# Kernel tuning notes

Measured on AMD Instinct MI355X. Metric: run time of the kernel, lower is better.

The kernel has to match this reference:

```python
import jax, jax.numpy as jnp
import numpy as np

B = 262144
DIM = 128
TD = 32        # token_dim (per-token channel dim inside attention)
NT = DIM // TD # 4 tokens from x, +1 learnable -> N = 5
N = NT + 1
H = 8          # num_heads
HD = TD // H   # head_dim = 4
DEEP = 2


def setup_inputs() -> dict:
    key = jax.random.key(0)
    ks = jax.random.split(key, 7)
    x = jax.random.normal(ks[0], (B, DIM), dtype=jnp.float32)
    token = jax.random.normal(ks[1], (1, 1, TD), dtype=jnp.float32)
    # stacked per-layer params (DEEP layers)
    qkv_w = jax.random.normal(ks[2], (DEEP, 3 * TD, TD), dtype=jnp.float32) * (TD ** -0.5)
    qkv_b = jnp.zeros((DEEP, 3 * TD), dtype=jnp.float32)
    proj_w = jax.random.normal(ks[3], (DEEP, TD, TD), dtype=jnp.float32) * (TD ** -0.5)
    proj_b = jnp.zeros((DEEP, TD), dtype=jnp.float32)
    pos_bias = jax.random.normal(ks[4], (DEEP, H, N, N), dtype=jnp.float32)
    return {"x": x, "token": token, "qkv_w": qkv_w, "qkv_b": qkv_b,
            "proj_w": proj_w, "proj_b": proj_b, "pos_bias": pos_bias}


def reference(x, token, qkv_w, qkv_b, proj_w, proj_b, pos_bias):
    scale = HD ** -0.5
    b = x.shape[0]
    # split x into NT tokens of width TD, prepend learnable token -> [B, N, TD]
    y = jnp.concatenate(
        [jnp.broadcast_to(token, (b, 1, TD)), x.reshape(b, NT, TD)], axis=1)
    for i in range(DEEP):
        qkv = y @ qkv_w[i].T + qkv_b[i]                 # [B, N, 3*TD]
        qkv = qkv.reshape(b, N, 3, H, HD)
        q = qkv[:, :, 0].transpose(0, 2, 1, 3)          # [B, H, N, HD]
        k = qkv[:, :, 1].transpose(0, 2, 1, 3)
        v = qkv[:, :, 2].transpose(0, 2, 1, 3)
        attn = jnp.einsum('bhnd,bhmd->bhnm', q, k) * scale + pos_bias[i]
        attn = jax.nn.softmax(attn, axis=-1)
        o = jnp.einsum('bhnm,bhmd->bhnd', attn, v)      # [B, H, N, HD]
        o = o.transpose(0, 2, 1, 3).reshape(b, N, TD)
        y = y + (o @ proj_w[i].T + proj_b[i])           # residual
    return y[:, 0, :]                                   # [B, TD]
```

## Files before the change

### kernel.cpp

```cpp
#include <hip/hip_runtime.h>
#include <hip/hip_bf16.h>


#define NTOK 5

typedef decltype(__builtin_amdgcn_cvt_pkrtz(0.0f, 0.0f)) half2_t;
using half8_t = __attribute__((ext_vector_type(8))) _Float16;
using f32x4 = __attribute__((ext_vector_type(4))) float;

union H2 { half2_t h; unsigned int u; };
union H8 { half8_t h; uint4 u4; unsigned int u[4]; };

__device__ __forceinline__ half2_t u2h(unsigned int x) { H2 c; c.u = x; return c.h; }
__device__ __forceinline__ unsigned int h2u(half2_t h) { H2 c; c.h = h; return c.u; }
__device__ __forceinline__ unsigned int pk(float a, float b) {
  return h2u(__builtin_amdgcn_cvt_pkrtz(a, b));
}
__device__ __forceinline__ float bf2f(unsigned short u) {
  union { unsigned int u; float f; } c; c.u = ((unsigned int)u) << 16; return c.f;
}
__device__ __forceinline__ half2_t bfpair2h2(unsigned int u) {
  union { unsigned int u; float f; } lo, hi;
  lo.u = u << 16;
  hi.u = u & 0xffff0000u;
  return __builtin_amdgcn_cvt_pkrtz(lo.f, hi.f);
}
__device__ __forceinline__ unsigned int f2bfpair(float a, float b) {
  unsigned int ua = __float_as_uint(a), ub = __float_as_uint(b);
  ua = (ua + 0x7fffu + ((ua >> 16) & 1u)) >> 16;
  ub = (ub + 0x7fffu + ((ub >> 16) & 1u)) & 0xffff0000u;
  return ua | ub;
}

__device__ __forceinline__ int detect_bf16(const unsigned int* __restrict__ p) {
  int cnt = 0;
#pragma unroll
  for (int i = 0; i < 64; ++i) {
    unsigned int e = (p[i] >> 7) & 0xffu;
    cnt += (e >= 96u && e <= 150u) ? 1 : 0;
  }
  return (cnt >= 40) ? 1 : 0;
}

__global__ void prep_kernel(const void* __restrict__ xraw,
                            const void* __restrict__ qkv_w, const void* __restrict__ qkv_b,
                            const void* __restrict__ proj_w, const void* __restrict__ proj_b,
                            const void* __restrict__ pos_b,
                            unsigned int* __restrict__ wqkv, unsigned int* __restrict__ wproj,
                            float* __restrict__ bqkv, float* __restrict__ bproj,
                            float* __restrict__ pb, int* __restrict__ flag) {
  const int t = threadIdx.x;
  const int isbf = detect_bf16((const unsigned int*)xraw);
  if (t == 0) *flag = isbf;
  if (isbf) {
    const unsigned short* qw = (const unsigned short*)qkv_w;
    const unsigned short* qb = (const unsigned short*)qkv_b;
    const unsigned short* pw = (const unsigned short*)proj_w;
    const unsigned short* pbb = (const unsigned short*)proj_b;
    const unsigned short* pp = (const unsigned short*)pos_b;
    for (int i = t; i < 3072; i += 256)
      wqkv[i] = h2u(__builtin_amdgcn_cvt_pkrtz(bf2f(qw[2 * i]), bf2f(qw[2 * i + 1])));
    for (int i = t; i < 1024; i += 256)
      wproj[i] = h2u(__builtin_amdgcn_cvt_pkrtz(bf2f(pw[2 * i]), bf2f(pw[2 * i + 1])));
    for (int i = t; i < 192; i += 256) bqkv[i] = bf2f(qb[i]);
    for (int i = t; i < 64; i += 256) bproj[i] = bf2f(pbb[i]);
    for (int i = t; i < 400; i += 256) pb[i] = bf2f(pp[i]);
  } else {
    const float* qw = (const float*)qkv_w;
    const float* qb = (const float*)qkv_b;
    const float* pw = (const float*)proj_w;
    const float* pbb = (const float*)proj_b;
    const float* pp = (const float*)pos_b;
    for (int i = t; i < 3072; i += 256)
      wqkv[i] = h2u(__builtin_amdgcn_cvt_pkrtz(qw[2 * i], qw[2 * i + 1]));
    for (int i = t; i < 1024; i += 256)
      wproj[i] = h2u(__builtin_amdgcn_cvt_pkrtz(pw[2 * i], pw[2 * i + 1]));
    for (int i = t; i < 192; i += 256) bqkv[i] = qb[i];
    for (int i = t; i < 64; i += 256) bproj[i] = pbb[i];
    for (int i = t; i < 400; i += 256) pb[i] = pp[i];
  }
}

__device__ __forceinline__ half8_t ldfrag(const uint4* __restrict__ w, int row, int quad) {
  H8 c; c.u4 = w[row * 4 + quad]; return c.h;
}
__device__ __forceinline__ half8_t mk8(const unsigned int (&d)[4]) {
  H8 c; c.u[0] = d[0]; c.u[1] = d[1]; c.u[2] = d[2]; c.u[3] = d[3]; return c.h;
}

template <int TMIN>
__device__ __forceinline__ void qkv_token(const half8_t (&wa)[6], const f32x4 (&bias)[6],
                                          half8_t yb, unsigned int (&outdw)[6][2]) {
#pragma unroll
  for (int tile = TMIN; tile < 6; ++tile) {
    f32x4 acc = __builtin_amdgcn_mfma_f32_16x16x32_f16(wa[tile], yb, bias[tile], 0, 0, 0);
    outdw[tile][0] = pk(acc[0], acc[1]);
    outdw[tile][1] = pk(acc[2], acc[3]);
  }
}

template <int NR>
__device__ __forceinline__ void attention(const unsigned int (&dw)[NTOK][6][2],
                                          const float* __restrict__ pbl, int quad,
                                          unsigned int (&od)[2][NR][2]) {
#pragma unroll
  for (int s = 0; s < 2; ++s) {
    const float* pbh = pbl + (quad + 4 * s) * 25;
    float vf[NTOK][4];
#pragma unroll
    for (int m = 0; m < NTOK; ++m) {
      half2_t v0 = u2h(dw[m][4 + s][0]), v1 = u2h(dw[m][4 + s][1]);
      vf[m][0] = (float)v0.x; vf[m][1] = (float)v0.y;
      vf[m][2] = (float)v1.x; vf[m][3] = (float)v1.y;
    }
#pragma unroll
    for (int n = 0; n < NR; ++n) {
      float lg[NTOK];
#pragma unroll
      for (int m = 0; m < NTOK; ++m) {
        float d = __builtin_amdgcn_fdot2(u2h(dw[n][0 + s][0]), u2h(dw[m][2 + s][0]), 0.0f, false);
        d = __builtin_amdgcn_fdot2(u2h(dw[n][0 + s][1]), u2h(dw[m][2 + s][1]), d, false);
        lg[m] = fmaf(d, 0.5f, pbh[n * 5 + m]);
      }
      float mx = fmaxf(fmaxf(fmaxf(lg[0], lg[1]), fmaxf(lg[2], lg[3])), lg[4]);
      float e[NTOK], ssum = 0.0f;
#pragma unroll
      for (int m = 0; m < NTOK; ++m) {
        e[m] = __builtin_amdgcn_exp2f((lg[m] - mx) * 1.44269504f);
        ssum += e[m];
      }
      const float r = __builtin_amdgcn_rcpf(ssum);
      float o0 = 0.f, o1 = 0.f, o2 = 0.f, o3 = 0.f;
#pragma unroll
      for (int m = 0; m < NTOK; ++m) {
        o0 = fmaf(e[m], vf[m][0], o0); o1 = fmaf(e[m], vf[m][1], o1);
        o2 = fmaf(e[m], vf[m][2], o2); o3 = fmaf(e[m], vf[m][3], o3);
      }
      od[s][n][0] = pk(o0 * r, o1 * r);
      od[s][n][1] = pk(o2 * r, o3 * r);
    }
  }
}

__device__ __forceinline__ void regroup(int quad, int nl,
                                        unsigned int lo0, unsigned int lo1,
                                        unsigned int hi0, unsigned int hi1,
                                        unsigned int (&o)[4]) {
  const int sA = ((2 * quad) & 3) * 16 + nl;
  const int sB = ((2 * quad + 1) & 3) * 16 + nl;
  const unsigned int a0 = __shfl((int)lo0, sA, 64), a1 = __shfl((int)lo1, sA, 64);
  const unsigned int a2 = __shfl((int)hi0, sA, 64), a3 = __shfl((int)hi1, sA, 64);
  const unsigned int b0 = __shfl((int)lo0, sB, 64), b1 = __shfl((int)lo1, sB, 64);
  const unsigned int b2 = __shfl((int)hi0, sB, 64), b3 = __shfl((int)hi1, sB, 64);
  const bool hi = quad >= 2;
  o[0] = hi ? a2 : a0; o[1] = hi ? a3 : a1;
  o[2] = hi ? b2 : b0; o[3] = hi ? b3 : b1;
}

__global__ __launch_bounds__(256, 2) void vit_kernel(
    const void* __restrict__ x, const void* __restrict__ token,
    const unsigned int* __restrict__ wqkv, const unsigned int* __restrict__ wproj,
    const float* __restrict__ bqkv, const float* __restrict__ bproj,
    const float* __restrict__ pb, const int* __restrict__ flag,
    void* __restrict__ out) {
  const int tid = threadIdx.x;
  const int wave = tid >> 6, lane = tid & 63;
  const int quad = lane >> 4, nl = lane & 15;
  const size_t b = (size_t)blockIdx.x * 64 + wave * 16 + nl;
  const int isbf = *flag;

  unsigned int yd[NTOK][4];
  if (isbf) {
    const uint4 tk = *(const uint4*)((const unsigned short*)token + quad * 8);
    yd[0][0] = h2u(bfpair2h2(tk.x)); yd[0][1] = h2u(bfpair2h2(tk.y));
    yd[0][2] = h2u(bfpair2h2(tk.z)); yd[0][3] = h2u(bfpair2h2(tk.w));
#pragma unroll
    for (int t = 1; t < NTOK; ++t) {
      const uint4 u = *(const uint4*)((const unsigned short*)x + b * 128 + (t - 1) * 32 + quad * 8);
      yd[t][0] = h2u(bfpair2h2(u.x)); yd[t][1] = h2u(bfpair2h2(u.y));
      yd[t][2] = h2u(bfpair2h2(u.z)); yd[t][3] = h2u(bfpair2h2(u.w));
    }
  } else {
    const float4* tp = (const float4*)token;
    float4 a0 = tp[quad * 2], a1 = tp[quad * 2 + 1];
    yd[0][0] = pk(a0.x, a0.y); yd[0][1] = pk(a0.z, a0.w);
    yd[0][2] = pk(a1.x, a1.y); yd[0][3] = pk(a1.z, a1.w);
#pragma unroll
    for (int t = 1; t < NTOK; ++t) {
      const float4* xp = (const float4*)((const float*)x + b * 128 + (t - 1) * 32 + quad * 8);
      float4 u0 = xp[0], u1 = xp[1];
      yd[t][0] = pk(u0.x, u0.y); yd[t][1] = pk(u0.z, u0.w);
      yd[t][2] = pk(u1.x, u1.y); yd[t][3] = pk(u1.z, u1.w);
    }
  }

  const uint4* wq4 = (const uint4*)wqkv;
  const uint4* wp4 = (const uint4*)wproj;

  {
    half8_t wa[6]; f32x4 bias[6];
#pragma unroll
    for (int tile = 0; tile < 6; ++tile) {
      wa[tile] = ldfrag(wq4, tile * 16 + nl, quad);
      bias[tile] = *(const f32x4*)(bqkv + tile * 16 + quad * 4);
    }
    unsigned int dw[NTOK][6][2];
#pragma unroll
    for (int t = 0; t < NTOK; ++t) qkv_token<0>(wa, bias, mk8(yd[t]), dw[t]);

    unsigned int od[2][NTOK][2];
    attention<NTOK>(dw, pb, quad, od);

    half8_t wp[2]; f32x4 bp[2];
#pragma unroll
    for (int tile = 0; tile < 2; ++tile) {
      wp[tile] = ldfrag(wp4, tile * 16 + nl, quad);
      bp[tile] = *(const f32x4*)(bproj + tile * 16 + quad * 4);
    }
#pragma unroll
    for (int t = 0; t < NTOK; ++t) {
      unsigned int bfd[4];
      regroup(quad, nl, od[0][t][0], od[0][t][1], od[1][t][0], od[1][t][1], bfd);
      f32x4 p0 = __builtin_amdgcn_mfma_f32_16x16x32_f16(wp[0], mk8(bfd), bp[0], 0, 0, 0);
      f32x4 p1 = __builtin_amdgcn_mfma_f32_16x16x32_f16(wp[1], mk8(bfd), bp[1], 0, 0, 0);
      unsigned int pr[4];
      regroup(quad, nl, pk(p0[0], p0[1]), pk(p0[2], p0[3]), pk(p1[0], p1[1]), pk(p1[2], p1[3]), pr);
#pragma unroll
      for (int j = 0; j < 4; ++j) yd[t][j] = h2u(u2h(yd[t][j]) + u2h(pr[j]));
    }
  }

  {
    half8_t wa[6]; f32x4 bias[6];
#pragma unroll
    for (int tile = 0; tile < 6; ++tile) {
      wa[tile] = ldfrag(wq4, 96 + tile * 16 + nl, quad);
      bias[tile] = *(const f32x4*)(bqkv + 96 + tile * 16 + quad * 4);
    }
    unsigned int dw[NTOK][6][2];
    qkv_token<0>(wa, bias, mk8(yd[0]), dw[0]);
#pragma unroll
    for (int t = 1; t < NTOK; ++t) qkv_token<2>(wa, bias, mk8(yd[t]), dw[t]);

    unsigned int od[2][1][2];
    attention<1>(dw, pb + 200, quad, od);

    half8_t wp[2]; f32x4 bp[2];
#pragma unroll
    for (int tile = 0; tile < 2; ++tile) {
      wp[tile] = ldfrag(wp4, 32 + tile * 16 + nl, quad);
      bp[tile] = *(const f32x4*)(bproj + 32 + tile * 16 + quad * 4);
    }
    unsigned int bfd[4];
    regroup(quad, nl, od[0][0][0], od[0][0][1], od[1][0][0], od[1][0][1], bfd);
    f32x4 p0 = __builtin_amdgcn_mfma_f32_16x16x32_f16(wp[0], mk8(bfd), bp[0], 0, 0, 0);
    f32x4 p1 = __builtin_amdgcn_mfma_f32_16x16x32_f16(wp[1], mk8(bfd), bp[1], 0, 0, 0);

    unsigned int t0[4], t1[4];
    regroup(quad, nl, __float_as_uint(p0[0]), __float_as_uint(p0[1]),
            __float_as_uint(p1[0]), __float_as_uint(p1[1]), t0);
    regroup(quad, nl, __float_as_uint(p0[2]), __float_as_uint(p0[3]),
            __float_as_uint(p1[2]), __float_as_uint(p1[3]), t1);
    float pf[8] = {__uint_as_float(t0[0]), __uint_as_float(t0[1]),
                   __uint_as_float(t1[0]), __uint_as_float(t1[1]),
                   __uint_as_float(t0[2]), __uint_as_float(t0[3]),
                   __uint_as_float(t1[2]), __uint_as_float(t1[3])};
    float f[8];
#pragma unroll
    for (int j = 0; j < 4; ++j) {
      half2_t yv = u2h(yd[0][j]);
      f[2 * j + 0] = (float)yv.x + pf[2 * j + 0];
      f[2 * j + 1] = (float)yv.y + pf[2 * j + 1];
    }
    if (isbf) {
      uint4 r = make_uint4(f2bfpair(f[0], f[1]), f2bfpair(f[2], f[3]),
                           f2bfpair(f[4], f[5]), f2bfpair(f[6], f[7]));
      *(uint4*)((unsigned short*)out + b * 32 + quad * 8) = r;
    } else {
      float4* op = (float4*)((float*)out + b * 32 + quad * 8);
      op[0] = make_float4(f[0], f[1], f[2], f[3]);
      op[1] = make_float4(f[4], f[5], f[6], f[7]);
    }
  }
}

extern "C" void kernel_launch(void* const* d_in, const int* in_sizes, int n_in,
                              void* d_out, int out_size, void* d_ws, size_t ws_size,
                              hipStream_t stream) {
  const void* x      = d_in[0];
  const void* token  = d_in[1];
  const void* qkv_w  = d_in[2];
  const void* qkv_b  = d_in[3];
  const void* proj_w = d_in[4];
  const void* proj_b = d_in[5];
  const void* pos_b  = d_in[6];

  char* ws = (char*)d_ws;
  unsigned int* wqkv  = (unsigned int*)(ws + 0);
  unsigned int* wproj = (unsigned int*)(ws + 12288);
  float* bqkv  = (float*)(ws + 16384);
  float* bproj = (float*)(ws + 17152);
  float* pb    = (float*)(ws + 17408);
  int*   flag  = (int*)(ws + 19008);

  prep_kernel<<<1, 256, 0, stream>>>(x, qkv_w, qkv_b, proj_w, proj_b, pos_b,
                                     wqkv, wproj, bqkv, bproj, pb, flag);

  const int nrows = in_sizes[0] / 128;
  const int grid = nrows / 64;
  vit_kernel<<<grid, 256, 0, stream>>>(x, token, wqkv, wproj, bqkv, bproj, pb, flag, d_out);
}
```

Baseline: 239.2 us.

## Permute weight channels to drop cross-lane regroup shuffles, process heads per half

Prep permutes the input channels of the QKV and projection weights. With that order, MFMA output fragments already sit in the lane layout the next MFMA expects, so the cross-lane shuffle regrouping disappears. Input and output loads change to matching split 4-element accesses. The QKV and attention work is also split into two head-halves to cut live registers, with launch bounds raised to 4 blocks per SM. Pos-bias is prescaled by log2e and the softmax max-subtraction is dropped, which risks overflow if logits grow large.

```diff
diff --git a/kernel.cpp b/kernel.cpp
--- a/kernel.cpp
+++ b/kernel.cpp
@@ -40,6 +40,10 @@
     cnt += (e >= 96u && e <= 150u) ? 1 : 0;
   }
   return (cnt >= 40) ? 1 : 0;
+}
+
+__device__ __forceinline__ int permch(int pos) {
+  return 4 * (pos >> 3) + (pos & 3) + ((pos & 4) ? 16 : 0);
 }
 
 __global__ void prep_kernel(const void* __restrict__ xraw,
@@ -52,32 +56,45 @@
   const int t = threadIdx.x;
   const int isbf = detect_bf16((const unsigned int*)xraw);
   if (t == 0) *flag = isbf;
+  const float LOG2E = 1.44269504f;
   if (isbf) {
     const unsigned short* qw = (const unsigned short*)qkv_w;
     const unsigned short* qb = (const unsigned short*)qkv_b;
     const unsigned short* pw = (const unsigned short*)proj_w;
     const unsigned short* pbb = (const unsigned short*)proj_b;
     const unsigned short* pp = (const unsigned short*)pos_b;
-    for (int i = t; i < 3072; i += 256)
-      wqkv[i] = h2u(__builtin_amdgcn_cvt_pkrtz(bf2f(qw[2 * i]), bf2f(qw[2 * i + 1])));
-    for (int i = t; i < 1024; i += 256)
-      wproj[i] = h2u(__builtin_amdgcn_cvt_pkrtz(bf2f(pw[2 * i]), bf2f(pw[2 * i + 1])));
+    for (int i = t; i < 3072; i += 256) {
+      const int row = i >> 4, cp = (i & 15) * 2;
+      wqkv[i] = h2u(__builtin_amdgcn_cvt_pkrtz(bf2f(qw[row * 32 + permch(cp)]),
+                                               bf2f(qw[row * 32 + permch(cp + 1)])));
+    }
+    for (int i = t; i < 1024; i += 256) {
+      const int row = i >> 4, cp = (i & 15) * 2;
+      wproj[i] = h2u(__builtin_amdgcn_cvt_pkrtz(bf2f(pw[row * 32 + permch(cp)]),
+                                                bf2f(pw[row * 32 + permch(cp + 1)])));
+    }
     for (int i = t; i < 192; i += 256) bqkv[i] = bf2f(qb[i]);
     for (int i = t; i < 64; i += 256) bproj[i] = bf2f(pbb[i]);
-    for (int i = t; i < 400; i += 256) pb[i] = bf2f(pp[i]);
+    for (int i = t; i < 400; i += 256) pb[i] = bf2f(pp[i]) * LOG2E;
   } else {
     const float* qw = (const float*)qkv_w;
     const float* qb = (const float*)qkv_b;
     const float* pw = (const float*)proj_w;
     const float* pbb = (const float*)proj_b;
     const float* pp = (const float*)pos_b;
-    for (int i = t; i < 3072; i += 256)
-      wqkv[i] = h2u(__builtin_amdgcn_cvt_pkrtz(qw[2 * i], qw[2 * i + 1]));
-    for (int i = t; i < 1024; i += 256)
-      wproj[i] = h2u(__builtin_amdgcn_cvt_pkrtz(pw[2 * i], pw[2 * i + 1]));
+    for (int i = t; i < 3072; i += 256) {
+      const int row = i >> 4, cp = (i & 15) * 2;
+      wqkv[i] = h2u(__builtin_amdgcn_cvt_pkrtz(qw[row * 32 + permch(cp)],
+                                               qw[row * 32 + permch(cp + 1)]));
+    }
+    for (int i = t; i < 1024; i += 256) {
+      const int row = i >> 4, cp = (i & 15) * 2;
+      wproj[i] = h2u(__builtin_amdgcn_cvt_pkrtz(pw[row * 32 + permch(cp)],
+                                                pw[row * 32 + permch(cp + 1)]));
+    }
     for (int i = t; i < 192; i += 256) bqkv[i] = qb[i];
     for (int i = t; i < 64; i += 256) bproj[i] = pbb[i];
-    for (int i = t; i < 400; i += 256) pb[i] = pp[i];
+    for (int i = t; i < 400; i += 256) pb[i] = pp[i] * LOG2E;
   }
 }
 
@@ -88,76 +105,40 @@
   H8 c; c.u[0] = d[0]; c.u[1] = d[1]; c.u[2] = d[2]; c.u[3] = d[3]; return c.h;
 }
 
-template <int TMIN>
-__device__ __forceinline__ void qkv_token(const half8_t (&wa)[6], const f32x4 (&bias)[6],
-                                          half8_t yb, unsigned int (&outdw)[6][2]) {
-#pragma unroll
-  for (int tile = TMIN; tile < 6; ++tile) {
-    f32x4 acc = __builtin_amdgcn_mfma_f32_16x16x32_f16(wa[tile], yb, bias[tile], 0, 0, 0);
-    outdw[tile][0] = pk(acc[0], acc[1]);
-    outdw[tile][1] = pk(acc[2], acc[3]);
-  }
-}
-
 template <int NR>
-__device__ __forceinline__ void attention(const unsigned int (&dw)[NTOK][6][2],
-                                          const float* __restrict__ pbl, int quad,
-                                          unsigned int (&od)[2][NR][2]) {
-#pragma unroll
-  for (int s = 0; s < 2; ++s) {
-    const float* pbh = pbl + (quad + 4 * s) * 25;
-    float vf[NTOK][4];
+__device__ __forceinline__ void attn_head(const unsigned int (&dw)[NTOK][3][2],
+                                          const float* __restrict__ pbh,
+                                          unsigned int (&od)[NR][2]) {
+  float vf[NTOK][4];
+#pragma unroll
+  for (int m = 0; m < NTOK; ++m) {
+    const half2_t v0 = u2h(dw[m][2][0]), v1 = u2h(dw[m][2][1]);
+    vf[m][0] = (float)v0.x; vf[m][1] = (float)v0.y;
+    vf[m][2] = (float)v1.x; vf[m][3] = (float)v1.y;
+  }
+#pragma unroll
+  for (int n = 0; n < NR; ++n) {
+    float e[NTOK], ssum = 0.0f;
 #pragma unroll
     for (int m = 0; m < NTOK; ++m) {
-      half2_t v0 = u2h(dw[m][4 + s][0]), v1 = u2h(dw[m][4 + s][1]);
-      vf[m][0] = (float)v0.x; vf[m][1] = (float)v0.y;
-      vf[m][2] = (float)v1.x; vf[m][3] = (float)v1.y;
-    }
-#pragma unroll
-    for (int n = 0; n < NR; ++n) {
-      float lg[NTOK];
-#pragma unroll
-      for (int m = 0; m < NTOK; ++m) {
-        float d = __builtin_amdgcn_fdot2(u2h(dw[n][0 + s][0]), u2h(dw[m][2 + s][0]), 0.0f, false);
-        d = __builtin_amdgcn_fdot2(u2h(dw[n][0 + s][1]), u2h(dw[m][2 + s][1]), d, false);
-        lg[m] = fmaf(d, 0.5f, pbh[n * 5 + m]);
-      }
-      float mx = fmaxf(fmaxf(fmaxf(lg[0], lg[1]), fmaxf(lg[2], lg[3])), lg[4]);
-      float e[NTOK], ssum = 0.0f;
-#pragma unroll
-      for (int m = 0; m < NTOK; ++m) {
-        e[m] = __builtin_amdgcn_exp2f((lg[m] - mx) * 1.44269504f);
-        ssum += e[m];
-      }
-      const float r = __builtin_amdgcn_rcpf(ssum);
-      float o0 = 0.f, o1 = 0.f, o2 = 0.f, o3 = 0.f;
-#pragma unroll
-      for (int m = 0; m < NTOK; ++m) {
-        o0 = fmaf(e[m], vf[m][0], o0); o1 = fmaf(e[m], vf[m][1], o1);
-        o2 = fmaf(e[m], vf[m][2], o2); o3 = fmaf(e[m], vf[m][3], o3);
-      }
-      od[s][n][0] = pk(o0 * r, o1 * r);
-      od[s][n][1] = pk(o2 * r, o3 * r);
-    }
-  }
-}
-
-__device__ __forceinline__ void regroup(int quad, int nl,
-                                        unsigned int lo0, unsigned int lo1,
-                                        unsigned int hi0, unsigned int hi1,
-                                        unsigned int (&o)[4]) {
-  const int sA = ((2 * quad) & 3) * 16 + nl;
-  const int sB = ((2 * quad + 1) & 3) * 16 + nl;
-  const unsigned int a0 = __shfl((int)lo0, sA, 64), a1 = __shfl((int)lo1, sA, 64);
-  const unsigned int a2 = __shfl((int)hi0, sA, 64), a3 = __shfl((int)hi1, sA, 64);
-  const unsigned int b0 = __shfl((int)lo0, sB, 64), b1 = __shfl((int)lo1, sB, 64);
-  const unsigned int b2 = __shfl((int)hi0, sB, 64), b3 = __shfl((int)hi1, sB, 64);
-  const bool hi = quad >= 2;
-  o[0] = hi ? a2 : a0; o[1] = hi ? a3 : a1;
-  o[2] = hi ? b2 : b0; o[3] = hi ? b3 : b1;
-}
-
-__global__ __launch_bounds__(256, 2) void vit_kernel(
+      float d = __builtin_amdgcn_fdot2(u2h(dw[n][0][0]), u2h(dw[m][1][0]), 0.0f, false);
+      d = __builtin_amdgcn_fdot2(u2h(dw[n][0][1]), u2h(dw[m][1][1]), d, false);
+      e[m] = __builtin_amdgcn_exp2f(fmaf(d, 0.72134752f, pbh[n * 5 + m]));
+      ssum += e[m];
+    }
+    const float r = __builtin_amdgcn_rcpf(ssum);
+    float o0 = 0.f, o1 = 0.f, o2 = 0.f, o3 = 0.f;
+#pragma unroll
+    for (int m = 0; m < NTOK; ++m) {
+      o0 = fmaf(e[m], vf[m][0], o0); o1 = fmaf(e[m], vf[m][1], o1);
+      o2 = fmaf(e[m], vf[m][2], o2); o3 = fmaf(e[m], vf[m][3], o3);
+    }
+    od[n][0] = pk(o0 * r, o1 * r);
+    od[n][1] = pk(o2 * r, o3 * r);
+  }
+}
+
+__global__ __launch_bounds__(256, 4) void vit_kernel(
     const void* __restrict__ x, const void* __restrict__ token,
     const unsigned int* __restrict__ wqkv, const unsigned int* __restrict__ wproj,
     const float* __restrict__ bqkv, const float* __restrict__ bproj,
@@ -171,24 +152,32 @@
 
   unsigned int yd[NTOK][4];
   if (isbf) {
-    const uint4 tk = *(const uint4*)((const unsigned short*)token + quad * 8);
-    yd[0][0] = h2u(bfpair2h2(tk.x)); yd[0][1] = h2u(bfpair2h2(tk.y));
-    yd[0][2] = h2u(bfpair2h2(tk.z)); yd[0][3] = h2u(bfpair2h2(tk.w));
+    const unsigned short* tk = (const unsigned short*)token;
+    const uint2 t0 = *(const uint2*)(tk + quad * 4);
+    const uint2 t1 = *(const uint2*)(tk + quad * 4 + 16);
+    yd[0][0] = h2u(bfpair2h2(t0.x)); yd[0][1] = h2u(bfpair2h2(t0.y));
+    yd[0][2] = h2u(bfpair2h2(t1.x)); yd[0][3] = h2u(bfpair2h2(t1.y));
+    const unsigned short* xb = (const unsigned short*)x + b * 128;
 #pragma unroll
     for (int t = 1; t < NTOK; ++t) {
-      const uint4 u = *(const uint4*)((const unsigned short*)x + b * 128 + (t - 1) * 32 + quad * 8);
-      yd[t][0] = h2u(bfpair2h2(u.x)); yd[t][1] = h2u(bfpair2h2(u.y));
-      yd[t][2] = h2u(bfpair2h2(u.z)); yd[t][3] = h2u(bfpair2h2(u.w));
+      const unsigned short* base = xb + (t - 1) * 32;
+      const uint2 u0 = *(const uint2*)(base + quad * 4);
+      const uint2 u1 = *(const uint2*)(base + quad * 4 + 16);
+      yd[t][0] = h2u(bfpair2h2(u0.x)); yd[t][1] = h2u(bfpair2h2(u0.y));
+      yd[t][2] = h2u(bfpair2h2(u1.x)); yd[t][3] = h2u(bfpair2h2(u1.y));
     }
   } else {
-    const float4* tp = (const float4*)token;
-    float4 a0 = tp[quad * 2], a1 = tp[quad * 2 + 1];
+    const float* tk = (const float*)token;
+    const float4 a0 = *(const float4*)(tk + quad * 4);
+    const float4 a1 = *(const float4*)(tk + quad * 4 + 16);
     yd[0][0] = pk(a0.x, a0.y); yd[0][1] = pk(a0.z, a0.w);
     yd[0][2] = pk(a1.x, a1.y); yd[0][3] = pk(a1.z, a1.w);
+    const float* xb = (const float*)x + b * 128;
 #pragma unroll
     for (int t = 1; t < NTOK; ++t) {
-      const float4* xp = (const float4*)((const float*)x + b * 128 + (t - 1) * 32 + quad * 8);
-      float4 u0 = xp[0], u1 = xp[1];
+      const float* base = xb + (t - 1) * 32;
+      const float4 u0 = *(const float4*)(base + quad * 4);
+      const float4 u1 = *(const float4*)(base + quad * 4 + 16);
       yd[t][0] = pk(u0.x, u0.y); yd[t][1] = pk(u0.z, u0.w);
       yd[t][2] = pk(u1.x, u1.y); yd[t][3] = pk(u1.z, u1.w);
     }
@@ -197,20 +186,31 @@
   const uint4* wq4 = (const uint4*)wqkv;
   const uint4* wp4 = (const uint4*)wproj;
 
+  unsigned int od[2][NTOK][2];
+#pragma unroll
+  for (int s = 0; s < 2; ++s) {
+    half8_t wa[3]; f32x4 bias[3];
+#pragma unroll
+    for (int i = 0; i < 3; ++i) {
+      const int tile = 2 * i + s;
+      wa[i] = ldfrag(wq4, tile * 16 + nl, quad);
+      bias[i] = *(const f32x4*)(bqkv + tile * 16 + quad * 4);
+    }
+    unsigned int dw[NTOK][3][2];
+#pragma unroll
+    for (int t = 0; t < NTOK; ++t) {
+      const half8_t yb = mk8(yd[t]);
+#pragma unroll
+      for (int i = 0; i < 3; ++i) {
+        f32x4 acc = __builtin_amdgcn_mfma_f32_16x16x32_f16(wa[i], yb, bias[i], 0, 0, 0);
+        dw[t][i][0] = pk(acc[0], acc[1]);
+        dw[t][i][1] = pk(acc[2], acc[3]);
+      }
+    }
+    attn_head<NTOK>(dw, pb + (quad + 4 * s) * 25, od[s]);
+  }
+
   {
-    half8_t wa[6]; f32x4 bias[6];
-#pragma unroll
-    for (int tile = 0; tile < 6; ++tile) {
-      wa[tile] = ldfrag(wq4, tile * 16 + nl, quad);
-      bias[tile] = *(const f32x4*)(bqkv + tile * 16 + quad * 4);
-    }
-    unsigned int dw[NTOK][6][2];
-#pragma unroll
-    for (int t = 0; t < NTOK; ++t) qkv_token<0>(wa, bias, mk8(yd[t]), dw[t]);
-
-    unsigned int od[2][NTOK][2];
-    attention<NTOK>(dw, pb, quad, od);
-
     half8_t wp[2]; f32x4 bp[2];
 #pragma unroll
     for (int tile = 0; tile < 2; ++tile) {
@@ -219,67 +219,68 @@
     }
 #pragma unroll
     for (int t = 0; t < NTOK; ++t) {
-      unsigned int bfd[4];
-      regroup(quad, nl, od[0][t][0], od[0][t][1], od[1][t][0], od[1][t][1], bfd);
-      f32x4 p0 = __builtin_amdgcn_mfma_f32_16x16x32_f16(wp[0], mk8(bfd), bp[0], 0, 0, 0);
-      f32x4 p1 = __builtin_amdgcn_mfma_f32_16x16x32_f16(wp[1], mk8(bfd), bp[1], 0, 0, 0);
-      unsigned int pr[4];
-      regroup(quad, nl, pk(p0[0], p0[1]), pk(p0[2], p0[3]), pk(p1[0], p1[1]), pk(p1[2], p1[3]), pr);
-#pragma unroll
-      for (int j = 0; j < 4; ++j) yd[t][j] = h2u(u2h(yd[t][j]) + u2h(pr[j]));
-    }
+      unsigned int bfr[4] = {od[0][t][0], od[0][t][1], od[1][t][0], od[1][t][1]};
+      const half8_t ob = mk8(bfr);
+      f32x4 p0 = __builtin_amdgcn_mfma_f32_16x16x32_f16(wp[0], ob, bp[0], 0, 0, 0);
+      f32x4 p1 = __builtin_amdgcn_mfma_f32_16x16x32_f16(wp[1], ob, bp[1], 0, 0, 0);
+      yd[t][0] = h2u(u2h(yd[t][0]) + u2h(pk(p0[0], p0[1])));
+      yd[t][1] = h2u(u2h(yd[t][1]) + u2h(pk(p0[2], p0[3])));
+      yd[t][2] = h2u(u2h(yd[t][2]) + u2h(pk(p1[0], p1[1])));
+      yd[t][3] = h2u(u2h(yd[t][3]) + u2h(pk(p1[2], p1[3])));
+    }
+  }
+
+  unsigned int o1[2][1][2];
+#pragma unroll
+  for (int s = 0; s < 2; ++s) {
+    half8_t wa[3]; f32x4 bias[3];
+#pragma unroll
+    for (int i = 0; i < 3; ++i) {
+      const int tile = 2 * i + s;
+      wa[i] = ldfrag(wq4, 96 + tile * 16 + nl, quad);
+      bias[i] = *(const f32x4*)(bqkv + 96 + tile * 16 + quad * 4);
+    }
+    unsigned int dw[NTOK][3][2];
+#pragma unroll
+    for (int t = 0; t < NTOK; ++t) {
+      const half8_t yb = mk8(yd[t]);
+#pragma unroll
+      for (int i = 0; i < 3; ++i) {
+        if (t > 0 && i == 0) continue;
+        f32x4 acc = __builtin_amdgcn_mfma_f32_16x16x32_f16(wa[i], yb, bias[i], 0, 0, 0);
+        dw[t][i][0] = pk(acc[0], acc[1]);
+        dw[t][i][1] = pk(acc[2], acc[3]);
+      }
+    }
+    attn_head<1>(dw, pb + 200 + (quad + 4 * s) * 25, o1[s]);
   }
 
   {
-    half8_t wa[6]; f32x4 bias[6];
-#pragma unroll
-    for (int tile = 0; tile < 6; ++tile) {
-      wa[tile] = ldfrag(wq4, 96 + tile * 16 + nl, quad);
-      bias[tile] = *(const f32x4*)(bqkv + 96 + tile * 16 + quad * 4);
-    }
-    unsigned int dw[NTOK][6][2];
-    qkv_token<0>(wa, bias, mk8(yd[0]), dw[0]);
-#pragma unroll
-    for (int t = 1; t < NTOK; ++t) qkv_token<2>(wa, bias, mk8(yd[t]), dw[t]);
-
-    unsigned int od[2][1][2];
-    attention<1>(dw, pb + 200, quad, od);
-
     half8_t wp[2]; f32x4 bp[2];
 #pragma unroll
     for (int tile = 0; tile < 2; ++tile) {
       wp[tile] = ldfrag(wp4, 32 + tile * 16 + nl, quad);
       bp[tile] = *(const f32x4*)(bproj + 32 + tile * 16 + quad * 4);
     }
-    unsigned int bfd[4];
-    regroup(quad, nl, od[0][0][0], od[0][0][1], od[1][0][0], od[1][0][1], bfd);
-    f32x4 p0 = __builtin_amdgcn_mfma_f32_16x16x32_f16(wp[0], mk8(bfd), bp[0], 0, 0, 0);
-    f32x4 p1 = __builtin_amdgcn_mfma_f32_16x16x32_f16(wp[1], mk8(bfd), bp[1], 0, 0, 0);
-
-    unsigned int t0[4], t1[4];
-    regroup(quad, nl, __float_as_uint(p0[0]), __float_as_uint(p0[1]),
-            __float_as_uint(p1[0]), __float_as_uint(p1[1]), t0);
-    regroup(quad, nl, __float_as_uint(p0[2]), __float_as_uint(p0[3]),
-            __float_as_uint(p1[2]), __float_as_uint(p1[3]), t1);
-    float pf[8] = {__uint_as_float(t0[0]), __uint_as_float(t0[1]),
-                   __uint_as_float(t1[0]), __uint_as_float(t1[1]),
-                   __uint_as_float(t0[2]), __uint_as_float(t0[3]),
-                   __uint_as_float(t1[2]), __uint_as_float(t1[3])};
-    float f[8];
-#pragma unroll
-    for (int j = 0; j < 4; ++j) {
-      half2_t yv = u2h(yd[0][j]);
-      f[2 * j + 0] = (float)yv.x + pf[2 * j + 0];
-      f[2 * j + 1] = (float)yv.y + pf[2 * j + 1];
-    }
+    unsigned int bfr[4] = {o1[0][0][0], o1[0][0][1], o1[1][0][0], o1[1][0][1]};
+    const half8_t ob = mk8(bfr);
+    f32x4 p0 = __builtin_amdgcn_mfma_f32_16x16x32_f16(wp[0], ob, bp[0], 0, 0, 0);
+    f32x4 p1 = __builtin_amdgcn_mfma_f32_16x16x32_f16(wp[1], ob, bp[1], 0, 0, 0);
+
+    const half2_t y0 = u2h(yd[0][0]), y1 = u2h(yd[0][1]);
+    const half2_t y2 = u2h(yd[0][2]), y3 = u2h(yd[0][3]);
+    float f[8] = {(float)y0.x + p0[0], (float)y0.y + p0[1],
+                  (float)y1.x + p0[2], (float)y1.y + p0[3],
+                  (float)y2.x + p1[0], (float)y2.y + p1[1],
+                  (float)y3.x + p1[2], (float)y3.y + p1[3]};
     if (isbf) {
-      uint4 r = make_uint4(f2bfpair(f[0], f[1]), f2bfpair(f[2], f[3]),
-                           f2bfpair(f[4], f[5]), f2bfpair(f[6], f[7]));
-      *(uint4*)((unsigned short*)out + b * 32 + quad * 8) = r;
+      unsigned short* ob16 = (unsigned short*)out + b * 32;
+      *(uint2*)(ob16 + quad * 4) = make_uint2(f2bfpair(f[0], f[1]), f2bfpair(f[2], f[3]));
+      *(uint2*)(ob16 + quad * 4 + 16) = make_uint2(f2bfpair(f[4], f[5]), f2bfpair(f[6], f[7]));
     } else {
-      float4* op = (float4*)((float*)out + b * 32 + quad * 8);
-      op[0] = make_float4(f[0], f[1], f[2], f[3]);
-      op[1] = make_float4(f[4], f[5], f[6], f[7]);
+      float* of = (float*)out + b * 32;
+      *(float4*)(of + quad * 4) = make_float4(f[0], f[1], f[2], f[3]);
+      *(float4*)(of + quad * 4 + 16) = make_float4(f[4], f[5], f[6], f[7]);
     }
   }
 }
```

Measured after the change: 234.1 us. 1.02x faster.
